# Optimization experiments

Measured on AMD Instinct MI355X. Metric: run time of the kernel, lower is better.

Reference implementation:

```python
import jax, jax.numpy as jnp
import numpy as np

D_MODEL = 1024
N_HEAD = 16
HEAD_DIM = D_MODEL // N_HEAD


def setup_inputs() -> dict:
    key = jax.random.key(0)
    ks = jax.random.split(key, 11)
    B, L = 1, 2048
    s = 1.0 / np.sqrt(D_MODEL)
    return {
        "q": jax.random.normal(ks[0], (B, L, D_MODEL), jnp.float32),
        "k": jax.random.normal(ks[1], (B, L, D_MODEL), jnp.float32),
        "v": jax.random.normal(ks[2], (B, L, D_MODEL), jnp.float32),
        "w_q": jax.random.normal(ks[3], (D_MODEL, D_MODEL), jnp.float32) * s,
        "b_q": jax.random.normal(ks[4], (D_MODEL,), jnp.float32) * s,
        "w_k": jax.random.normal(ks[5], (D_MODEL, D_MODEL), jnp.float32) * s,
        "b_k": jax.random.normal(ks[6], (D_MODEL,), jnp.float32) * s,
        "w_v": jax.random.normal(ks[7], (D_MODEL, D_MODEL), jnp.float32) * s,
        "b_v": jax.random.normal(ks[8], (D_MODEL,), jnp.float32) * s,
        "w_o": jax.random.normal(ks[9], (D_MODEL, D_MODEL), jnp.float32) * s,
        "b_o": jax.random.normal(ks[10], (D_MODEL,), jnp.float32) * s,
    }


def _split_heads(x):
    # [B, L, D] -> [B, H, L, Dh]
    B, L, D = x.shape
    return x.reshape(B, L, N_HEAD, HEAD_DIM).transpose(0, 2, 1, 3)


def reference(q, k, v, w_q, b_q, w_k, b_k, w_v, b_v, w_o, b_o):
    # Linear projections (torch Linear: x @ W.T + b; here weights stored as [D_in, D_out])
    qh = _split_heads(q @ w_q + b_q)
    kh = _split_heads(k @ w_k + b_k)
    vh = _split_heads(v @ w_v + b_v)
    scale = 1.0 / jnp.sqrt(jnp.asarray(HEAD_DIM, qh.dtype))
    # [B, H, Lq, Lk] full score matrix (faithful to naive implementation)
    score = jnp.einsum("bhqd,bhkd->bhqk", qh, kh) * scale
    attn = jax.nn.softmax(score, axis=-1)
    out = jnp.einsum("bhqk,bhkd->bhqd", attn, vh)
    # concat heads: [B, H, L, Dh] -> [B, L, D]
    B, H, L, Dh = out.shape
    out = out.transpose(0, 2, 1, 3).reshape(B, L, H * Dh)
    return out @ w_o + b_o  # dropout p=0.0 -> identity
```

## Files before the change

kernel.cpp:

```cpp
#include <hip/hip_runtime.h>
#include <hip/hip_bf16.h>
#include <stdint.h>
#include <stddef.h>

typedef __bf16 bf16_t;
typedef __bf16 v8bf __attribute__((ext_vector_type(8)));
typedef __bf16 v4bf __attribute__((ext_vector_type(4)));
typedef float  v4f  __attribute__((ext_vector_type(4)));

#define L_SEQ 2048
#define DM    1024
#define NH    16
#define LOG2E 1.44269504088896340736f
#define SCL   (0.125f * LOG2E)

__device__ __forceinline__ void async_cp16(const void* g, void* l) {
  __builtin_amdgcn_global_load_lds(
      (__attribute__((address_space(1))) void*)(g),
      (__attribute__((address_space(3))) void*)(l),
      16, 0, 0);
}

__device__ __forceinline__ v4f mfma16(v8bf a, v8bf b, v4f c) {
  return __builtin_amdgcn_mfma_f32_16x16x32_bf16(a, b, c, 0, 0, 0);
}

#if __has_builtin(__builtin_amdgcn_exp2f)
__device__ __forceinline__ float fast_exp2(float x) { return __builtin_amdgcn_exp2f(x); }
#else
__device__ __forceinline__ float fast_exp2(float x) { return exp2f(x); }
#endif

__global__ void k_prep(
    const float* __restrict__ q, const float* __restrict__ k,
    const float* __restrict__ v,
    const float* __restrict__ w0, const float* __restrict__ w1,
    const float* __restrict__ w2, const float* __restrict__ w3,
    bf16_t* __restrict__ Qb, bf16_t* __restrict__ Kb, bf16_t* __restrict__ Vb,
    bf16_t* __restrict__ o0, bf16_t* __restrict__ o1,
    bf16_t* __restrict__ o2, bf16_t* __restrict__ o3)
{
  const int z = blockIdx.z;
  const int tid = threadIdx.x;
  if (z < 4) {
    const float* in = (z == 0) ? w0 : (z == 1) ? w1 : (z == 2) ? w2 : w3;
    bf16_t*     out = (z == 0) ? o0 : (z == 1) ? o1 : (z == 2) ? o2 : o3;
    __shared__ float t[64 * 65];
    const int r0 = blockIdx.y * 64, c0 = blockIdx.x * 64;
#pragma unroll
    for (int p = 0; p < 16; ++p) {
      const int idx = p * 256 + tid;
      const int r = idx >> 6, c = idx & 63;
      t[r * 65 + c] = in[(size_t)(r0 + r) * DM + c0 + c];
    }
    __syncthreads();
#pragma unroll
    for (int p = 0; p < 4; ++p) {
      const int idx = p * 256 + tid;
      const int c  = idx >> 4;
      const int r4 = (idx & 15) * 4;
      v4bf y;
#pragma unroll
      for (int j = 0; j < 4; ++j) y[j] = (bf16_t)t[(r4 + j) * 65 + c];
      *(v4bf*)(&out[(size_t)(c0 + c) * DM + r0 + r4]) = y;
    }
  } else {
    const float* src = (z == 4) ? q : (z == 5) ? k : v;
    bf16_t*      dst = (z == 4) ? Qb : (z == 5) ? Kb : Vb;
    const int n4 = (L_SEQ * DM) / 4;
    const int base = (blockIdx.y * 16 + blockIdx.x) * 256 + tid;
#pragma unroll
    for (int i = base; i < n4; i += 16 * 16 * 256) {
      v4f x = ((const v4f*)src)[i];
      v4bf y;
      y[0] = (bf16_t)x[0]; y[1] = (bf16_t)x[1];
      y[2] = (bf16_t)x[2]; y[3] = (bf16_t)x[3];
      ((v4bf*)dst)[i] = y;
    }
  }
}

template <int MI, typename OutT>
__device__ __forceinline__ void gemm_body(
    const bf16_t* __restrict__ A, const bf16_t* __restrict__ Bt,
    const float* __restrict__ biasN, const float* __restrict__ biasM,
    OutT* __restrict__ C, int M, int N, int K, int bx, int by)
{
  constexpr int BM = MI * 32;
  __shared__ __align__(16) bf16_t As[2][BM * 64];
  __shared__ __align__(16) bf16_t Bs[2][64 * 64];
  const int tid  = threadIdx.x;
  const int w    = tid >> 6;
  const int lane = tid & 63;
  const int l16  = lane & 15;
  const int q4   = lane >> 4;
  const int m0   = by * BM, n0 = bx * 64;
  const int wm   = (w >> 1) * (MI * 16), wn = (w & 1) * 32;
  const int lr = lane >> 3, lc = lane & 7;

  v4f acc[MI][2];
#pragma unroll
  for (int i = 0; i < MI; ++i)
#pragma unroll
    for (int j = 0; j < 2; ++j) {
      v4f z = {0.f, 0.f, 0.f, 0.f};
      acc[i][j] = z;
    }

  auto stage = [&](int k0, int buf) {
#pragma unroll
    for (int c = 0; c < MI; ++c) {
      const int row = (BM / 4) * w + 8 * c + lr;
      const int q   = lc ^ (row & 7);
      async_cp16(A + (size_t)(m0 + row) * K + k0 + q * 8,
                 &As[buf][((BM / 4) * w + 8 * c) * 64]);
    }
#pragma unroll
    for (int c = 0; c < 2; ++c) {
      const int row = 16 * w + 8 * c + lr;
      const int q   = lc ^ (row & 7);
      async_cp16(Bt + (size_t)(n0 + row) * K + k0 + q * 8,
                 &Bs[buf][(16 * w + 8 * c) * 64]);
    }
  };

  stage(0, 0);
  __syncthreads();

  const int nk = K >> 6;
  for (int kt = 0; kt < nk; ++kt) {
    if (kt + 1 < nk) stage((kt + 1) << 6, (kt + 1) & 1);
    const int buf = kt & 1;
#pragma unroll
    for (int ks = 0; ks < 2; ++ks) {
      v8bf af[MI], bf_[2];
#pragma unroll
      for (int mi = 0; mi < MI; ++mi) {
        const int row = wm + mi * 16 + l16;
        const int pc  = (4 * ks + q4) ^ (row & 7);
        af[mi] = *(const v8bf*)(&As[buf][row * 64 + pc * 8]);
      }
#pragma unroll
      for (int ni = 0; ni < 2; ++ni) {
        const int row = wn + ni * 16 + l16;
        const int pc  = (4 * ks + q4) ^ (row & 7);
        bf_[ni] = *(const v8bf*)(&Bs[buf][row * 64 + pc * 8]);
      }
#pragma unroll
      for (int mi = 0; mi < MI; ++mi)
#pragma unroll
        for (int ni = 0; ni < 2; ++ni)
          acc[mi][ni] = mfma16(af[mi], bf_[ni], acc[mi][ni]);
    }
    __syncthreads();
  }

  float bvn[2] = {0.f, 0.f};
  if (biasN) {
#pragma unroll
    for (int ni = 0; ni < 2; ++ni) bvn[ni] = biasN[n0 + wn + ni * 16 + l16];
  }
#pragma unroll
  for (int mi = 0; mi < MI; ++mi) {
#pragma unroll
    for (int r = 0; r < 4; ++r) {
      const int row = m0 + wm + mi * 16 + q4 * 4 + r;
      const float bm = biasM ? biasM[row] : 0.f;
#pragma unroll
      for (int ni = 0; ni < 2; ++ni) {
        const int col = n0 + wn + ni * 16 + l16;
        C[(size_t)row * N + col] = (OutT)(acc[mi][ni][r] + bvn[ni] + bm);
      }
    }
  }
}

__global__ __launch_bounds__(256, 3) void k_gemm_fused(
    const bf16_t* __restrict__ Qb, const bf16_t* __restrict__ Kb,
    const bf16_t* __restrict__ Vb,
    const bf16_t* __restrict__ Wqkt,
    const bf16_t* __restrict__ Wvt,
    const float* __restrict__ bq, const float* __restrict__ bk,
    const float* __restrict__ bv,
    bf16_t* __restrict__ QKo, bf16_t* __restrict__ Vtr)
{
  const int idx = blockIdx.x;
  const bf16_t *A, *Bt;
  const float *bN = nullptr, *bM = nullptr;
  bf16_t* C;
  int M, N, bx, by;
  if (idx < 512) {
    by = idx & 15; bx = idx >> 4;
    A  = (bx < 16) ? Qb : Kb;
    Bt = Wqkt;
    bN = (bx < 16) ? bq : (bk - DM);
    C  = QKo; M = L_SEQ; N = 2 * DM;
  } else {
    const int i2 = idx - 512;
    by = i2 & 7; bx = i2 >> 3;
    A  = Wvt; Bt = Vb; bM = bv;
    C  = Vtr; M = DM; N = L_SEQ;
  }
  gemm_body<4, bf16_t>(A, Bt, bN, bM, C, M, N, DM, bx, by);
}

__global__ __launch_bounds__(256, 2) void k_gemm_oproj(
    const bf16_t* __restrict__ A, const bf16_t* __restrict__ Bt,
    const float* __restrict__ bias, float* __restrict__ C)
{
  gemm_body<2, float>(A, Bt, bias, nullptr, C, L_SEQ, DM, DM,
                      blockIdx.x, blockIdx.y);
}

__global__ __launch_bounds__(256, 2) void k_attn(
    const bf16_t* __restrict__ QKp,
    const bf16_t* __restrict__ Vt,
    bf16_t* __restrict__ AO)
{
  constexpr int LD = 2 * DM;
  const int lid = blockIdx.x;
  const int hd  = (lid & 7) + 8 * ((lid >> 3) & 1);
  const int q0  = (lid >> 4) * 64;
  const int tid = threadIdx.x, w = tid >> 6, lane = tid & 63;
  const int l16 = lane & 15, q4 = lane >> 4;
  const int lr8 = lane >> 3, lc8 = lane & 7;

  __shared__ __align__(16) char smem_raw[81920];
  bf16_t* Ks = (bf16_t*)smem_raw;
  bf16_t* Vs = (bf16_t*)(smem_raw + 32768);
  bf16_t* QP = (bf16_t*)(smem_raw + 65536);
  float* Ored = (float*)smem_raw;
  float* Lred = (float*)(smem_raw + 69632);

  const bf16_t* Qp = QKp;
  const bf16_t* Kp = QKp + DM;

  const bf16_t* pK[4];
#pragma unroll
  for (int c = 0; c < 4; ++c) {
    const int row = 32 * w + 8 * c + lr8;
    const int g   = lc8 ^ (row & 7);
    pK[c] = Kp + (size_t)row * LD + hd * 64 + g * 8;
  }
  const bf16_t* pV[4];
#pragma unroll
  for (int c = 0; c < 4; ++c) {
    const int row = 16 * w + 4 * c + q4;
    const int g   = l16 ^ (row & 15);
    pV[c] = Vt + (size_t)(hd * 64 + row) * L_SEQ + g * 8;
  }
  auto stage_kv = [&](int j0, int db) {
#pragma unroll
    for (int c = 0; c < 4; ++c)
      async_cp16(pK[c] + (size_t)j0 * LD, Ks + db * (128 * 64) + (32 * w + 8 * c) * 64);
#pragma unroll
    for (int c = 0; c < 4; ++c)
      async_cp16(pV[c] + j0, Vs + db * (64 * 128) + (16 * w + 4 * c) * 128);
  };

#pragma unroll
  for (int c = 0; c < 2; ++c) {
    const int row = 16 * w + 8 * c + lr8;
    const int g   = lc8 ^ (row & 7);
    async_cp16(Qp + (size_t)(q0 + row) * LD + hd * 64 + g * 8,
               QP + (16 * w + 8 * c) * 64);
  }
  stage_kv(0, 0);
  __syncthreads();

  v8bf bq[4][2];
#pragma unroll
  for (int qg = 0; qg < 4; ++qg)
#pragma unroll
    for (int ks = 0; ks < 2; ++ks) {
      const int row = qg * 16 + l16;
      const int pc  = (4 * ks + q4) ^ (row & 7);
      bq[qg][ks] = *(const v8bf*)(&QP[row * 64 + pc * 8]);
    }
  __syncthreads();

  bf16_t* Pw = QP + w * (64 * 32);

  float l_acc[4] = {0.f, 0.f, 0.f, 0.f};
  v4f od[4][4];
#pragma unroll
  for (int i = 0; i < 4; ++i)
#pragma unroll
    for (int j = 0; j < 4; ++j) { v4f z = {0.f, 0.f, 0.f, 0.f}; od[i][j] = z; }

  for (int rt = 0; rt < L_SEQ / 128; ++rt) {
    if (rt + 1 < L_SEQ / 128) stage_kv((rt + 1) * 128, (rt + 1) & 1);
    const bf16_t* Kt = Ks + (rt & 1) * (128 * 64);
    const bf16_t* Vv = Vs + (rt & 1) * (64 * 128);

    v4f st[2][4];
    __builtin_amdgcn_s_setprio(1);
#pragma unroll
    for (int jf = 0; jf < 2; ++jf) {
#pragma unroll
      for (int qg = 0; qg < 4; ++qg) { v4f z = {0.f, 0.f, 0.f, 0.f}; st[jf][qg] = z; }
#pragma unroll
      for (int ks = 0; ks < 2; ++ks) {
        const int rowk = 32 * w + jf * 16 + l16;
        const int pc   = (4 * ks + q4) ^ (rowk & 7);
        v8bf ak = *(const v8bf*)(&Kt[rowk * 64 + pc * 8]);
#pragma unroll
        for (int qg = 0; qg < 4; ++qg)
          st[jf][qg] = mfma16(ak, bq[qg][ks], st[jf][qg]);
      }
    }
    __builtin_amdgcn_s_setprio(0);

#pragma unroll
    for (int jf = 0; jf < 2; ++jf)
#pragma unroll
      for (int qg = 0; qg < 4; ++qg) {
        v4bf pb;
#pragma unroll
        for (int r = 0; r < 4; ++r) {
          const float p = fast_exp2(st[jf][qg][r] * SCL);
          l_acc[qg] += p;
          pb[r] = (bf16_t)p;
        }
        const int q    = qg * 16 + l16;
        const int cch  = jf * 2 + (q4 >> 1);
        const int phys = cch ^ (q & 3);
        *(v4bf*)(&Pw[q * 32 + phys * 8 + (q4 & 1) * 4]) = pb;
      }

    __builtin_amdgcn_s_setprio(1);
    v8bf av[4];
#pragma unroll
    for (int dd = 0; dd < 4; ++dd) {
      const int rowv = dd * 16 + l16;
      const int pv   = (4 * w + q4) ^ (rowv & 15);
      av[dd] = *(const v8bf*)(&Vv[rowv * 128 + pv * 8]);
    }
#pragma unroll
    for (int qg = 0; qg < 4; ++qg) {
      const int q    = qg * 16 + l16;
      const int phys = q4 ^ (q & 3);
      v8bf bp = *(const v8bf*)(&Pw[q * 32 + phys * 8]);
#pragma unroll
      for (int dd = 0; dd < 4; ++dd)
        od[dd][qg] = mfma16(av[dd], bp, od[dd][qg]);
    }
    __builtin_amdgcn_s_setprio(0);
    __syncthreads();
  }

  float* Ow = Ored + w * (64 * 68);
#pragma unroll
  for (int dd = 0; dd < 4; ++dd)
#pragma unroll
    for (int qg = 0; qg < 4; ++qg) {
      const int q  = qg * 16 + l16;
      const int d0 = dd * 16 + q4 * 4;
      *(v4f*)(&Ow[q * 68 + d0]) = od[dd][qg];
    }
#pragma unroll
  for (int qg = 0; qg < 4; ++qg) {
    float t = l_acc[qg];
    t += __shfl_xor(t, 16, 64);
    t += __shfl_xor(t, 32, 64);
    if (q4 == 0) Lred[w * 64 + qg * 16 + l16] = t;
  }
  __syncthreads();

  const int qq = 16 * w + (lane >> 2);
  const int d0 = (lane & 3) * 16;
  const float linv =
      1.f / (Lred[qq] + Lred[64 + qq] + Lred[128 + qq] + Lred[192 + qq]);
  float o[16];
#pragma unroll
  for (int c = 0; c < 4; ++c) {
    v4f t = *(const v4f*)(&Ored[qq * 68 + d0 + c * 4]);
#pragma unroll
    for (int e = 0; e < 4; ++e) o[c * 4 + e] = t[e];
  }
#pragma unroll
  for (int w2 = 1; w2 < 4; ++w2)
#pragma unroll
    for (int c = 0; c < 4; ++c) {
      v4f t = *(const v4f*)(&Ored[w2 * (64 * 68) + qq * 68 + d0 + c * 4]);
#pragma unroll
      for (int e = 0; e < 4; ++e) o[c * 4 + e] += t[e];
    }
  v8bf ob0, ob1;
#pragma unroll
  for (int e = 0; e < 8; ++e) ob0[e] = (bf16_t)(o[e] * linv);
#pragma unroll
  for (int e = 0; e < 8; ++e) ob1[e] = (bf16_t)(o[8 + e] * linv);
  bf16_t* dst = &AO[(size_t)(q0 + qq) * DM + hd * 64 + d0];
  *(v8bf*)(dst)     = ob0;
  *(v8bf*)(dst + 8) = ob1;
}

extern "C" void kernel_launch(void* const* d_in, const int* in_sizes, int n_in,
                              void* d_out, int out_size, void* d_ws, size_t ws_size,
                              hipStream_t stream)
{
  const float* q  = (const float*)d_in[0];
  const float* k  = (const float*)d_in[1];
  const float* v  = (const float*)d_in[2];
  const float* wq = (const float*)d_in[3];
  const float* bq = (const float*)d_in[4];
  const float* wk = (const float*)d_in[5];
  const float* bk = (const float*)d_in[6];
  const float* wv = (const float*)d_in[7];
  const float* bv = (const float*)d_in[8];
  const float* wo = (const float*)d_in[9];
  const float* bo = (const float*)d_in[10];
  float* out = (float*)d_out;

  const size_t SZ = (size_t)L_SEQ * DM;
  bf16_t* ws   = (bf16_t*)d_ws;
  bf16_t* Qb   = ws;
  bf16_t* Kb   = Qb + SZ;
  bf16_t* Vb   = Kb + SZ;
  bf16_t* QK   = Vb + SZ;
  bf16_t* Vtr  = QK + 2 * SZ;
  bf16_t* AO   = Vtr + SZ;
  bf16_t* Wqt  = AO + SZ;
  bf16_t* Wkt  = Wqt + (size_t)DM * DM;
  bf16_t* Wvt  = Wkt + (size_t)DM * DM;
  bf16_t* Wot  = Wvt + (size_t)DM * DM;

  k_prep<<<dim3(16, 16, 7), 256, 0, stream>>>(q, k, v, wq, wk, wv, wo,
                                              Qb, Kb, Vb, Wqt, Wkt, Wvt, Wot);
  k_gemm_fused<<<dim3(768), 256, 0, stream>>>(Qb, Kb, Vb, Wqt, Wvt,
                                              bq, bk, bv, QK, Vtr);
  k_attn<<<dim3(512), 256, 0, stream>>>(QK, Vtr, AO);
  k_gemm_oproj<<<dim3(16, 32), 256, 0, stream>>>(AO, Wot, bo, out);
}
```

Measured before the change: 168.7 us.

## Merge projection, attention and output GEMMs into one persistent kernel with grid barriers

Replaces three launches (fused QKV GEMM, attention, output projection) with one 512-block persistent kernel that uses atomic-counter grid barriers between stages. The GEMM tiles are rebalanced to a 128-wide N dimension so that each stage maps onto exactly 512 blocks, and shared memory is reused across stages. The aim is to remove inter-kernel launch gaps and tail effects. In exchange it depends on all 512 blocks being co-resident (two per CU), and the spin barriers add overhead and deadlock risk if occupancy drops.

```diff
diff --git a/kernel.cpp b/kernel.cpp
--- a/kernel.cpp
+++ b/kernel.cpp
@@ -13,6 +13,7 @@
 #define NH    16
 #define LOG2E 1.44269504088896340736f
 #define SCL   (0.125f * LOG2E)
+#define NBLK  512
 
 __device__ __forceinline__ void async_cp16(const void* g, void* l) {
   __builtin_amdgcn_global_load_lds(
@@ -30,6 +31,20 @@
 #else
 __device__ __forceinline__ float fast_exp2(float x) { return exp2f(x); }
 #endif
+
+__device__ __forceinline__ void gbar(int* cnt, int* gen) {
+  __threadfence();
+  __syncthreads();
+  if (threadIdx.x == 0) {
+    if (atomicAdd(cnt, 1) == NBLK - 1) {
+      __hip_atomic_store(gen, 1, __ATOMIC_RELEASE, __HIP_MEMORY_SCOPE_AGENT);
+    } else {
+      while (!__hip_atomic_load(gen, __ATOMIC_ACQUIRE, __HIP_MEMORY_SCOPE_AGENT))
+        __builtin_amdgcn_s_sleep(2);
+    }
+  }
+  __syncthreads();
+}
 
 __global__ void k_prep(
     const float* __restrict__ q, const float* __restrict__ k,
@@ -38,7 +53,8 @@
     const float* __restrict__ w2, const float* __restrict__ w3,
     bf16_t* __restrict__ Qb, bf16_t* __restrict__ Kb, bf16_t* __restrict__ Vb,
     bf16_t* __restrict__ o0, bf16_t* __restrict__ o1,
-    bf16_t* __restrict__ o2, bf16_t* __restrict__ o3)
+    bf16_t* __restrict__ o2, bf16_t* __restrict__ o3,
+    int* __restrict__ ctrl)
 {
   const int z = blockIdx.z;
   const int tid = threadIdx.x;
@@ -65,6 +81,7 @@
       *(v4bf*)(&out[(size_t)(c0 + c) * DM + r0 + r4]) = y;
     }
   } else {
+    if (z == 4 && blockIdx.x == 0 && blockIdx.y == 0 && tid < 32) ctrl[tid] = 0;
     const float* src = (z == 4) ? q : (z == 5) ? k : v;
     bf16_t*      dst = (z == 4) ? Qb : (z == 5) ? Kb : Vb;
     const int n4 = (L_SEQ * DM) / 4;
@@ -80,29 +97,30 @@
   }
 }
 
-template <int MI, typename OutT>
+template <int MI, int NI, typename OutT>
 __device__ __forceinline__ void gemm_body(
     const bf16_t* __restrict__ A, const bf16_t* __restrict__ Bt,
     const float* __restrict__ biasN, const float* __restrict__ biasM,
-    OutT* __restrict__ C, int M, int N, int K, int bx, int by)
+    OutT* __restrict__ C, int N, int K, int bx, int by, char* smem)
 {
   constexpr int BM = MI * 32;
-  __shared__ __align__(16) bf16_t As[2][BM * 64];
-  __shared__ __align__(16) bf16_t Bs[2][64 * 64];
+  constexpr int BN = NI * 32;
+  bf16_t* As = (bf16_t*)smem;
+  bf16_t* Bs = As + 2 * BM * 64;
   const int tid  = threadIdx.x;
   const int w    = tid >> 6;
   const int lane = tid & 63;
   const int l16  = lane & 15;
   const int q4   = lane >> 4;
-  const int m0   = by * BM, n0 = bx * 64;
-  const int wm   = (w >> 1) * (MI * 16), wn = (w & 1) * 32;
+  const int m0   = by * BM, n0 = bx * BN;
+  const int wm   = (w >> 1) * (MI * 16), wn = (w & 1) * (NI * 16);
   const int lr = lane >> 3, lc = lane & 7;
 
-  v4f acc[MI][2];
+  v4f acc[MI][NI];
 #pragma unroll
   for (int i = 0; i < MI; ++i)
 #pragma unroll
-    for (int j = 0; j < 2; ++j) {
+    for (int j = 0; j < NI; ++j) {
       v4f z = {0.f, 0.f, 0.f, 0.f};
       acc[i][j] = z;
     }
@@ -111,16 +129,16 @@
 #pragma unroll
     for (int c = 0; c < MI; ++c) {
       const int row = (BM / 4) * w + 8 * c + lr;
-      const int q   = lc ^ (row & 7);
-      async_cp16(A + (size_t)(m0 + row) * K + k0 + q * 8,
-                 &As[buf][((BM / 4) * w + 8 * c) * 64]);
-    }
-#pragma unroll
-    for (int c = 0; c < 2; ++c) {
-      const int row = 16 * w + 8 * c + lr;
-      const int q   = lc ^ (row & 7);
-      async_cp16(Bt + (size_t)(n0 + row) * K + k0 + q * 8,
-                 &Bs[buf][(16 * w + 8 * c) * 64]);
+      const int g   = lc ^ (row & 7);
+      async_cp16(A + (size_t)(m0 + row) * K + k0 + g * 8,
+                 &As[buf * (BM * 64) + ((BM / 4) * w + 8 * c) * 64]);
+    }
+#pragma unroll
+    for (int c = 0; c < NI; ++c) {
+      const int row = (BN / 4) * w + 8 * c + lr;
+      const int g   = lc ^ (row & 7);
+      async_cp16(Bt + (size_t)(n0 + row) * K + k0 + g * 8,
+                 &Bs[buf * (BN * 64) + ((BN / 4) * w + 8 * c) * 64]);
     }
   };
 
@@ -133,33 +151,32 @@
     const int buf = kt & 1;
 #pragma unroll
     for (int ks = 0; ks < 2; ++ks) {
-      v8bf af[MI], bf_[2];
+      v8bf af[MI], bf_[NI];
 #pragma unroll
       for (int mi = 0; mi < MI; ++mi) {
         const int row = wm + mi * 16 + l16;
         const int pc  = (4 * ks + q4) ^ (row & 7);
-        af[mi] = *(const v8bf*)(&As[buf][row * 64 + pc * 8]);
+        af[mi] = *(const v8bf*)(&As[buf * (BM * 64) + row * 64 + pc * 8]);
       }
 #pragma unroll
-      for (int ni = 0; ni < 2; ++ni) {
+      for (int ni = 0; ni < NI; ++ni) {
         const int row = wn + ni * 16 + l16;
         const int pc  = (4 * ks + q4) ^ (row & 7);
-        bf_[ni] = *(const v8bf*)(&Bs[buf][row * 64 + pc * 8]);
+        bf_[ni] = *(const v8bf*)(&Bs[buf * (BN * 64) + row * 64 + pc * 8]);
       }
 #pragma unroll
       for (int mi = 0; mi < MI; ++mi)
 #pragma unroll
-        for (int ni = 0; ni < 2; ++ni)
+        for (int ni = 0; ni < NI; ++ni)
           acc[mi][ni] = mfma16(af[mi], bf_[ni], acc[mi][ni]);
     }
     __syncthreads();
   }
 
-  float bvn[2] = {0.f, 0.f};
-  if (biasN) {
-#pragma unroll
-    for (int ni = 0; ni < 2; ++ni) bvn[ni] = biasN[n0 + wn + ni * 16 + l16];
-  }
+  float bvn[NI];
+#pragma unroll
+  for (int ni = 0; ni < NI; ++ni)
+    bvn[ni] = biasN ? biasN[n0 + wn + ni * 16 + l16] : 0.f;
 #pragma unroll
   for (int mi = 0; mi < MI; ++mi) {
 #pragma unroll
@@ -167,7 +184,7 @@
       const int row = m0 + wm + mi * 16 + q4 * 4 + r;
       const float bm = biasM ? biasM[row] : 0.f;
 #pragma unroll
-      for (int ni = 0; ni < 2; ++ni) {
+      for (int ni = 0; ni < NI; ++ni) {
         const int col = n0 + wn + ni * 16 + l16;
         C[(size_t)row * N + col] = (OutT)(acc[mi][ni][r] + bvn[ni] + bm);
       }
@@ -175,57 +192,19 @@
   }
 }
 
-__global__ __launch_bounds__(256, 3) void k_gemm_fused(
-    const bf16_t* __restrict__ Qb, const bf16_t* __restrict__ Kb,
-    const bf16_t* __restrict__ Vb,
-    const bf16_t* __restrict__ Wqkt,
-    const bf16_t* __restrict__ Wvt,
-    const float* __restrict__ bq, const float* __restrict__ bk,
-    const float* __restrict__ bv,
-    bf16_t* __restrict__ QKo, bf16_t* __restrict__ Vtr)
-{
-  const int idx = blockIdx.x;
-  const bf16_t *A, *Bt;
-  const float *bN = nullptr, *bM = nullptr;
-  bf16_t* C;
-  int M, N, bx, by;
-  if (idx < 512) {
-    by = idx & 15; bx = idx >> 4;
-    A  = (bx < 16) ? Qb : Kb;
-    Bt = Wqkt;
-    bN = (bx < 16) ? bq : (bk - DM);
-    C  = QKo; M = L_SEQ; N = 2 * DM;
-  } else {
-    const int i2 = idx - 512;
-    by = i2 & 7; bx = i2 >> 3;
-    A  = Wvt; Bt = Vb; bM = bv;
-    C  = Vtr; M = DM; N = L_SEQ;
-  }
-  gemm_body<4, bf16_t>(A, Bt, bN, bM, C, M, N, DM, bx, by);
-}
-
-__global__ __launch_bounds__(256, 2) void k_gemm_oproj(
-    const bf16_t* __restrict__ A, const bf16_t* __restrict__ Bt,
-    const float* __restrict__ bias, float* __restrict__ C)
-{
-  gemm_body<2, float>(A, Bt, bias, nullptr, C, L_SEQ, DM, DM,
-                      blockIdx.x, blockIdx.y);
-}
-
-__global__ __launch_bounds__(256, 2) void k_attn(
+__device__ __forceinline__ void attn_body(
+    int lid, char* smem_raw,
     const bf16_t* __restrict__ QKp,
     const bf16_t* __restrict__ Vt,
     bf16_t* __restrict__ AO)
 {
   constexpr int LD = 2 * DM;
-  const int lid = blockIdx.x;
   const int hd  = (lid & 7) + 8 * ((lid >> 3) & 1);
   const int q0  = (lid >> 4) * 64;
   const int tid = threadIdx.x, w = tid >> 6, lane = tid & 63;
   const int l16 = lane & 15, q4 = lane >> 4;
   const int lr8 = lane >> 3, lc8 = lane & 7;
 
-  __shared__ __align__(16) char smem_raw[81920];
   bf16_t* Ks = (bf16_t*)smem_raw;
   bf16_t* Vs = (bf16_t*)(smem_raw + 32768);
   bf16_t* QP = (bf16_t*)(smem_raw + 65536);
@@ -394,6 +373,42 @@
   bf16_t* dst = &AO[(size_t)(q0 + qq) * DM + hd * 64 + d0];
   *(v8bf*)(dst)     = ob0;
   *(v8bf*)(dst + 8) = ob1;
+}
+
+__global__ __launch_bounds__(256, 2) void k_mega(
+    const bf16_t* __restrict__ Qb, const bf16_t* __restrict__ Kb,
+    const bf16_t* __restrict__ Vb,
+    const bf16_t* __restrict__ Wqkt,
+    const bf16_t* __restrict__ Wvt,
+    const bf16_t* __restrict__ Wot,
+    const float* __restrict__ bq, const float* __restrict__ bk,
+    const float* __restrict__ bv, const float* __restrict__ bo,
+    bf16_t* __restrict__ QK, bf16_t* __restrict__ Vtr,
+    bf16_t* __restrict__ AO, float* __restrict__ out,
+    int* __restrict__ ctrl)
+{
+  __shared__ __align__(16) char smem[81920];
+  const int bid = blockIdx.x;
+
+  if (bid < 256) {
+    const int by = bid & 15, bx = bid >> 4;
+    const bf16_t* A  = (bx < 8) ? Qb : Kb;
+    const float*  bN = (bx < 8) ? bq : (bk - DM);
+    gemm_body<4, 4, bf16_t>(A, Wqkt, bN, nullptr, QK, 2 * DM, DM, bx, by, smem);
+  } else {
+    const int i2 = bid - 256;
+    const int by = i2 & 15, bx = i2 >> 4;
+    gemm_body<2, 4, bf16_t>(Wvt, Vb, nullptr, bv, Vtr, L_SEQ, DM, bx, by, smem);
+  }
+  gbar(ctrl + 0, ctrl + 1);
+
+  attn_body(bid, smem, QK, Vtr, AO);
+  gbar(ctrl + 2, ctrl + 3);
+
+  {
+    const int by = bid & 31, bx = bid >> 5;
+    gemm_body<2, 2, float>(AO, Wot, bo, nullptr, out, DM, DM, bx, by, smem);
+  }
 }
 
 extern "C" void kernel_launch(void* const* d_in, const int* in_sizes, int n_in,
@@ -425,11 +440,12 @@
   bf16_t* Wkt  = Wqt + (size_t)DM * DM;
   bf16_t* Wvt  = Wkt + (size_t)DM * DM;
   bf16_t* Wot  = Wvt + (size_t)DM * DM;
+  int*    ctrl = (int*)(Wot + (size_t)DM * DM);
 
   k_prep<<<dim3(16, 16, 7), 256, 0, stream>>>(q, k, v, wq, wk, wv, wo,
-                                              Qb, Kb, Vb, Wqt, Wkt, Wvt, Wot);
-  k_gemm_fused<<<dim3(768), 256, 0, stream>>>(Qb, Kb, Vb, Wqt, Wvt,
-                                              bq, bk, bv, QK, Vtr);
-  k_attn<<<dim3(512), 256, 0, stream>>>(QK, Vtr, AO);
-  k_gemm_oproj<<<dim3(16, 32), 256, 0, stream>>>(AO, Wot, bo, out);
-}
+                                              Qb, Kb, Vb, Wqt, Wkt, Wvt, Wot,
+                                              ctrl);
+  k_mega<<<dim3(NBLK), 256, 0, stream>>>(Qb, Kb, Vb, Wqt, Wvt, Wot,
+                                         bq, bk, bv, bo,
+                                         QK, Vtr, AO, out, ctrl);
+}
```

New measurement: 354.7 us. 2.1x slower.

## Halve attention query tile, load V directly from global, raise occupancy

Applied to the files above, without the earlier changes.

The attention kernel now handles 32 queries per block instead of 64, which doubles the grid to 1024 blocks. V fragments are read straight from global memory into registers each iteration rather than staged through LDS, so shared memory per block drops from 80KB to 40KB. Launch bounds rise to 4 blocks per SM. The aim is more parallelism and occupancy. In exchange, each block rereads K and V for half as many queries, doubling K/V global traffic, and the direct V loads are uncoalesced and may expose latency.

```diff
diff --git a/kernel.cpp b/kernel.cpp
--- a/kernel.cpp
+++ b/kernel.cpp
@@ -111,15 +111,15 @@
 #pragma unroll
     for (int c = 0; c < MI; ++c) {
       const int row = (BM / 4) * w + 8 * c + lr;
-      const int q   = lc ^ (row & 7);
-      async_cp16(A + (size_t)(m0 + row) * K + k0 + q * 8,
+      const int g   = lc ^ (row & 7);
+      async_cp16(A + (size_t)(m0 + row) * K + k0 + g * 8,
                  &As[buf][((BM / 4) * w + 8 * c) * 64]);
     }
 #pragma unroll
     for (int c = 0; c < 2; ++c) {
       const int row = 16 * w + 8 * c + lr;
-      const int q   = lc ^ (row & 7);
-      async_cp16(Bt + (size_t)(n0 + row) * K + k0 + q * 8,
+      const int g   = lc ^ (row & 7);
+      async_cp16(Bt + (size_t)(n0 + row) * K + k0 + g * 8,
                  &Bs[buf][(16 * w + 8 * c) * 64]);
     }
   };
@@ -212,7 +212,7 @@
                       blockIdx.x, blockIdx.y);
 }
 
-__global__ __launch_bounds__(256, 2) void k_attn(
+__global__ __launch_bounds__(256, 4) void k_attn(
     const bf16_t* __restrict__ QKp,
     const bf16_t* __restrict__ Vt,
     bf16_t* __restrict__ AO)
@@ -220,17 +220,16 @@
   constexpr int LD = 2 * DM;
   const int lid = blockIdx.x;
   const int hd  = (lid & 7) + 8 * ((lid >> 3) & 1);
-  const int q0  = (lid >> 4) * 64;
+  const int q0  = (lid >> 4) * 32;
   const int tid = threadIdx.x, w = tid >> 6, lane = tid & 63;
   const int l16 = lane & 15, q4 = lane >> 4;
   const int lr8 = lane >> 3, lc8 = lane & 7;
 
-  __shared__ __align__(16) char smem_raw[81920];
+  __shared__ __align__(16) char smem_raw[40960];
   bf16_t* Ks = (bf16_t*)smem_raw;
-  bf16_t* Vs = (bf16_t*)(smem_raw + 32768);
-  bf16_t* QP = (bf16_t*)(smem_raw + 65536);
+  bf16_t* QP = (bf16_t*)(smem_raw + 32768);
   float* Ored = (float*)smem_raw;
-  float* Lred = (float*)(smem_raw + 69632);
+  float* Lred = (float*)(smem_raw + 34816);
 
   const bf16_t* Qp = QKp;
   const bf16_t* Kp = QKp + DM;
@@ -242,35 +241,30 @@
     const int g   = lc8 ^ (row & 7);
     pK[c] = Kp + (size_t)row * LD + hd * 64 + g * 8;
   }
+  auto stage_k = [&](int j0, int db) {
+#pragma unroll
+    for (int c = 0; c < 4; ++c)
+      async_cp16(pK[c] + (size_t)j0 * LD,
+                 Ks + db * (128 * 64) + (32 * w + 8 * c) * 64);
+  };
+
   const bf16_t* pV[4];
 #pragma unroll
-  for (int c = 0; c < 4; ++c) {
-    const int row = 16 * w + 4 * c + q4;
-    const int g   = l16 ^ (row & 15);
-    pV[c] = Vt + (size_t)(hd * 64 + row) * L_SEQ + g * 8;
-  }
-  auto stage_kv = [&](int j0, int db) {
-#pragma unroll
-    for (int c = 0; c < 4; ++c)
-      async_cp16(pK[c] + (size_t)j0 * LD, Ks + db * (128 * 64) + (32 * w + 8 * c) * 64);
-#pragma unroll
-    for (int c = 0; c < 4; ++c)
-      async_cp16(pV[c] + j0, Vs + db * (64 * 128) + (16 * w + 4 * c) * 128);
-  };
-
-#pragma unroll
-  for (int c = 0; c < 2; ++c) {
-    const int row = 16 * w + 8 * c + lr8;
+  for (int dd = 0; dd < 4; ++dd)
+    pV[dd] = Vt + (size_t)(hd * 64 + dd * 16 + l16) * L_SEQ + 32 * w + q4 * 8;
+
+  {
+    const int row = 8 * w + lr8;
     const int g   = lc8 ^ (row & 7);
     async_cp16(Qp + (size_t)(q0 + row) * LD + hd * 64 + g * 8,
-               QP + (16 * w + 8 * c) * 64);
-  }
-  stage_kv(0, 0);
+               QP + (8 * w) * 64);
+  }
+  stage_k(0, 0);
   __syncthreads();
 
-  v8bf bq[4][2];
-#pragma unroll
-  for (int qg = 0; qg < 4; ++qg)
+  v8bf bq[2][2];
+#pragma unroll
+  for (int qg = 0; qg < 2; ++qg)
 #pragma unroll
     for (int ks = 0; ks < 2; ++ks) {
       const int row = qg * 16 + l16;
@@ -279,33 +273,35 @@
     }
   __syncthreads();
 
-  bf16_t* Pw = QP + w * (64 * 32);
-
-  float l_acc[4] = {0.f, 0.f, 0.f, 0.f};
-  v4f od[4][4];
+  bf16_t* Pw = QP + w * (32 * 32);
+
+  float l_acc[2] = {0.f, 0.f};
+  v4f od[4][2];
 #pragma unroll
   for (int i = 0; i < 4; ++i)
 #pragma unroll
-    for (int j = 0; j < 4; ++j) { v4f z = {0.f, 0.f, 0.f, 0.f}; od[i][j] = z; }
+    for (int j = 0; j < 2; ++j) { v4f z = {0.f, 0.f, 0.f, 0.f}; od[i][j] = z; }
 
   for (int rt = 0; rt < L_SEQ / 128; ++rt) {
-    if (rt + 1 < L_SEQ / 128) stage_kv((rt + 1) * 128, (rt + 1) & 1);
+    v8bf av[4];
+#pragma unroll
+    for (int dd = 0; dd < 4; ++dd) av[dd] = *(const v8bf*)(pV[dd] + rt * 128);
+    if (rt + 1 < L_SEQ / 128) stage_k((rt + 1) * 128, (rt + 1) & 1);
     const bf16_t* Kt = Ks + (rt & 1) * (128 * 64);
-    const bf16_t* Vv = Vs + (rt & 1) * (64 * 128);
-
-    v4f st[2][4];
+
+    v4f st[2][2];
     __builtin_amdgcn_s_setprio(1);
 #pragma unroll
     for (int jf = 0; jf < 2; ++jf) {
 #pragma unroll
-      for (int qg = 0; qg < 4; ++qg) { v4f z = {0.f, 0.f, 0.f, 0.f}; st[jf][qg] = z; }
+      for (int qg = 0; qg < 2; ++qg) { v4f z = {0.f, 0.f, 0.f, 0.f}; st[jf][qg] = z; }
 #pragma unroll
       for (int ks = 0; ks < 2; ++ks) {
         const int rowk = 32 * w + jf * 16 + l16;
         const int pc   = (4 * ks + q4) ^ (rowk & 7);
         v8bf ak = *(const v8bf*)(&Kt[rowk * 64 + pc * 8]);
 #pragma unroll
-        for (int qg = 0; qg < 4; ++qg)
+        for (int qg = 0; qg < 2; ++qg)
           st[jf][qg] = mfma16(ak, bq[qg][ks], st[jf][qg]);
       }
     }
@@ -314,7 +310,7 @@
 #pragma unroll
     for (int jf = 0; jf < 2; ++jf)
 #pragma unroll
-      for (int qg = 0; qg < 4; ++qg) {
+      for (int qg = 0; qg < 2; ++qg) {
         v4bf pb;
 #pragma unroll
         for (int r = 0; r < 4; ++r) {
@@ -329,15 +325,8 @@
       }
 
     __builtin_amdgcn_s_setprio(1);
-    v8bf av[4];
-#pragma unroll
-    for (int dd = 0; dd < 4; ++dd) {
-      const int rowv = dd * 16 + l16;
-      const int pv   = (4 * w + q4) ^ (rowv & 15);
-      av[dd] = *(const v8bf*)(&Vv[rowv * 128 + pv * 8]);
-    }
-#pragma unroll
-    for (int qg = 0; qg < 4; ++qg) {
+#pragma unroll
+    for (int qg = 0; qg < 2; ++qg) {
       const int q    = qg * 16 + l16;
       const int phys = q4 ^ (q & 3);
       v8bf bp = *(const v8bf*)(&Pw[q * 32 + phys * 8]);
@@ -349,31 +338,31 @@
     __syncthreads();
   }
 
-  float* Ow = Ored + w * (64 * 68);
+  float* Ow = Ored + w * (32 * 68);
 #pragma unroll
   for (int dd = 0; dd < 4; ++dd)
 #pragma unroll
-    for (int qg = 0; qg < 4; ++qg) {
+    for (int qg = 0; qg < 2; ++qg) {
       const int q  = qg * 16 + l16;
       const int d0 = dd * 16 + q4 * 4;
       *(v4f*)(&Ow[q * 68 + d0]) = od[dd][qg];
     }
 #pragma unroll
-  for (int qg = 0; qg < 4; ++qg) {
+  for (int qg = 0; qg < 2; ++qg) {
     float t = l_acc[qg];
     t += __shfl_xor(t, 16, 64);
     t += __shfl_xor(t, 32, 64);
-    if (q4 == 0) Lred[w * 64 + qg * 16 + l16] = t;
+    if (q4 == 0) Lred[w * 32 + qg * 16 + l16] = t;
   }
   __syncthreads();
 
-  const int qq = 16 * w + (lane >> 2);
-  const int d0 = (lane & 3) * 16;
+  const int qq = 8 * w + (lane >> 3);
+  const int d0 = (lane & 7) * 8;
   const float linv =
-      1.f / (Lred[qq] + Lred[64 + qq] + Lred[128 + qq] + Lred[192 + qq]);
-  float o[16];
-#pragma unroll
-  for (int c = 0; c < 4; ++c) {
+      1.f / (Lred[qq] + Lred[32 + qq] + Lred[64 + qq] + Lred[96 + qq]);
+  float o[8];
+#pragma unroll
+  for (int c = 0; c < 2; ++c) {
     v4f t = *(const v4f*)(&Ored[qq * 68 + d0 + c * 4]);
 #pragma unroll
     for (int e = 0; e < 4; ++e) o[c * 4 + e] = t[e];
@@ -381,19 +370,15 @@
 #pragma unroll
   for (int w2 = 1; w2 < 4; ++w2)
 #pragma unroll
-    for (int c = 0; c < 4; ++c) {
-      v4f t = *(const v4f*)(&Ored[w2 * (64 * 68) + qq * 68 + d0 + c * 4]);
+    for (int c = 0; c < 2; ++c) {
+      v4f t = *(const v4f*)(&Ored[w2 * (32 * 68) + qq * 68 + d0 + c * 4]);
 #pragma unroll
       for (int e = 0; e < 4; ++e) o[c * 4 + e] += t[e];
     }
-  v8bf ob0, ob1;
-#pragma unroll
-  for (int e = 0; e < 8; ++e) ob0[e] = (bf16_t)(o[e] * linv);
-#pragma unroll
-  for (int e = 0; e < 8; ++e) ob1[e] = (bf16_t)(o[8 + e] * linv);
-  bf16_t* dst = &AO[(size_t)(q0 + qq) * DM + hd * 64 + d0];
-  *(v8bf*)(dst)     = ob0;
-  *(v8bf*)(dst + 8) = ob1;
+  v8bf ob;
+#pragma unroll
+  for (int e = 0; e < 8; ++e) ob[e] = (bf16_t)(o[e] * linv);
+  *(v8bf*)(&AO[(size_t)(q0 + qq) * DM + hd * 64 + d0]) = ob;
 }
 
 extern "C" void kernel_launch(void* const* d_in, const int* in_sizes, int n_in,
@@ -430,6 +415,6 @@
                                               Qb, Kb, Vb, Wqt, Wkt, Wvt, Wot);
   k_gemm_fused<<<dim3(768), 256, 0, stream>>>(Qb, Kb, Vb, Wqt, Wvt,
                                               bq, bk, bv, QK, Vtr);
-  k_attn<<<dim3(512), 256, 0, stream>>>(QK, Vtr, AO);
+  k_attn<<<dim3(1024), 256, 0, stream>>>(QK, Vtr, AO);
   k_gemm_oproj<<<dim3(16, 32), 256, 0, stream>>>(AO, Wot, bo, out);
 }
```

New measurement: 179.6 us. 1.06x slower.
